# Optimization experiments

Hardware: AMD Instinct MI355X
Metric: run time of the kernel (lower is better)

The kernel has to match this reference:

```python
import jax, jax.numpy as jnp
import numpy as np

B, T, C, H = 2, 2048, 2048, 16
HD = C // H  # head_dim = 128


def setup_inputs() -> dict:
    key = jax.random.key(0)
    k1, k2, k3 = jax.random.split(key, 3)
    x = jax.random.normal(k1, (B, T, C), dtype=jnp.float32)
    # causal mask: positions with mask==0 are blocked (masked_fill(mask==0, -inf))
    mask = jnp.tril(jnp.ones((T, T), dtype=bool))[None, None]  # [1,1,T,T]
    W_qkv = jax.random.normal(k2, (C, 3 * C), dtype=jnp.float32) * (C ** -0.5)
    W_proj = jax.random.normal(k3, (C, C), dtype=jnp.float32) * (C ** -0.5)
    b_proj = jnp.zeros((C,), dtype=jnp.float32)
    return {"x": x, "mask": mask, "W_qkv": W_qkv, "W_proj": W_proj, "b_proj": b_proj}


def reference(x, mask, W_qkv, W_proj, b_proj):
    # QKV projection (Linear, bias=False)
    qkv = jnp.einsum('btc,cd->btd', x, W_qkv)            # [B,T,3C]
    qkv = qkv.reshape(B, T, 3, H, HD)
    q = qkv[:, :, 0].transpose(0, 2, 1, 3)               # [B,H,T,HD]
    k = qkv[:, :, 1].transpose(0, 2, 1, 3)
    v = qkv[:, :, 2].transpose(0, 2, 1, 3)
    # scaled dot-product attention (dropout is identity in eval)
    att = jnp.einsum('bhqd,bhkd->bhqk', q, k) / jnp.sqrt(jnp.float32(HD))
    att = jnp.where(mask, att, -jnp.inf)
    att = jax.nn.softmax(att, axis=-1)
    y = jnp.einsum('bhqk,bhkd->bhqd', att, v)            # [B,H,T,HD]
    y = y.transpose(0, 2, 1, 3).reshape(B, T, C)
    return jnp.einsum('btc,cd->btd', y, W_proj) + b_proj
```

## Files before the change

### kernel.cpp

```cpp
#include <hip/hip_runtime.h>
#include <hip/hip_bf16.h>

#define B_  2
#define T_  2048
#define C_  2048
#define H_  16
#define HD_ 128

using bf16x8 = __attribute__((ext_vector_type(8))) __bf16;
using f32x4  = __attribute__((ext_vector_type(4))) float;

__device__ __forceinline__ unsigned short f2bs(float f) {
    __hip_bfloat16 h = __float2bfloat16(f);
    return __builtin_bit_cast(unsigned short, h);
}

__device__ __forceinline__ void gload_lds16(const unsigned short* g, unsigned short* l) {
    __builtin_amdgcn_global_load_lds(
        (const __attribute__((address_space(1))) unsigned int*)g,
        (__attribute__((address_space(3))) unsigned int*)l, 16, 0, 0);
}

__global__ __launch_bounds__(256) void k_prep(const float* __restrict__ x,
                                              unsigned short* __restrict__ XB,
                                              const float* __restrict__ Wqkv,
                                              unsigned short* __restrict__ WQKVT,
                                              const float* __restrict__ Wproj,
                                              unsigned short* __restrict__ WPROJT) {
    __shared__ unsigned short t[64][65];
    int blk = blockIdx.x;
    int tid = threadIdx.x;
    if (blk < 8192) {
        int i = blk * 256 + tid;
        float4 v = reinterpret_cast<const float4*>(x)[i];
        ushort4 o;
        o.x = f2bs(v.x); o.y = f2bs(v.y); o.z = f2bs(v.z); o.w = f2bs(v.w);
        reinterpret_cast<ushort4*>(XB)[i] = o;
        return;
    }
    const float* in;
    unsigned short* out;
    int K = 2048, N, bx, by;
    if (blk < 11264) {
        in = Wqkv; out = WQKVT; N = 6144;
        bx = (blk - 8192) % 96; by = (blk - 8192) / 96;
    } else {
        in = Wproj; out = WPROJT; N = 2048;
        bx = (blk - 11264) % 32; by = (blk - 11264) / 32;
    }
    int k0 = by * 64, n0 = bx * 64;
#pragma unroll
    for (int p = 0; p < 4; ++p) {
        int idx = p * 256 + tid;
        int r = idx >> 4, c = (idx & 15) << 2;
        float4 v = *reinterpret_cast<const float4*>(in + (long)(k0 + r) * N + n0 + c);
        t[r][c] = f2bs(v.x); t[r][c + 1] = f2bs(v.y);
        t[r][c + 2] = f2bs(v.z); t[r][c + 3] = f2bs(v.w);
    }
    __syncthreads();
#pragma unroll
    for (int p = 0; p < 4; ++p) {
        int idx = p * 256 + tid;
        int r = idx >> 4, c = (idx & 15) << 2;
        ushort4 o;
        o.x = t[c][r]; o.y = t[c + 1][r]; o.z = t[c + 2][r]; o.w = t[c + 3][r];
        *reinterpret_cast<ushort4*>(out + (long)(n0 + r) * K + k0 + c) = o;
    }
}

template <int MODE>
__global__ __launch_bounds__(256, 2) void k_gemm(const unsigned short* __restrict__ A,
                                                 const unsigned short* __restrict__ Bt,
                                                 int M, int N, int K,
                                                 unsigned short* __restrict__ qkv,
                                                 float* __restrict__ out,
                                                 const float* __restrict__ bias) {
    __shared__ __align__(16) unsigned short lA[2][128 * 32];
    __shared__ __align__(16) unsigned short lB[2][128 * 32];

    int tid = threadIdx.x;
    int wave = tid >> 6, lane = tid & 63;
    int quad = lane >> 4, l16 = lane & 15;
    int wr = (wave >> 1) * 64, wc = (wave & 1) * 64;
    int m0 = blockIdx.y * 128, n0 = blockIdx.x * 128;

    int lrow = lane >> 2;
    int lcol = (lane & 3) << 3;
    const unsigned short* gA0 = A + (long)(m0 + wave * 32 + lrow) * K + lcol;
    const unsigned short* gA1 = A + (long)(m0 + wave * 32 + 16 + lrow) * K + lcol;
    const unsigned short* gB0 = Bt + (long)(n0 + wave * 32 + lrow) * K + lcol;
    const unsigned short* gB1 = Bt + (long)(n0 + wave * 32 + 16 + lrow) * K + lcol;
    int lofs0 = wave * 1024, lofs1 = wave * 1024 + 512;

    f32x4 zero = {0.f, 0.f, 0.f, 0.f};
    f32x4 acc[4][4];
#pragma unroll
    for (int i = 0; i < 4; ++i)
#pragma unroll
        for (int j = 0; j < 4; ++j) acc[i][j] = zero;

    for (int k0 = 0; k0 < K; k0 += 64) {
        __syncthreads();
#pragma unroll
        for (int h = 0; h < 2; ++h) {
            int kk = k0 + h * 32;
            gload_lds16(gA0 + kk, &lA[h][lofs0]);
            gload_lds16(gA1 + kk, &lA[h][lofs1]);
            gload_lds16(gB0 + kk, &lB[h][lofs0]);
            gload_lds16(gB1 + kk, &lB[h][lofs1]);
        }
        __syncthreads();
#pragma unroll
        for (int h = 0; h < 2; ++h) {
            bf16x8 af[4], bfr[4];
#pragma unroll
            for (int i = 0; i < 4; ++i)
                af[i] = *reinterpret_cast<const bf16x8*>(&lA[h][(wr + i * 16 + l16) * 32 + quad * 8]);
#pragma unroll
            for (int j = 0; j < 4; ++j)
                bfr[j] = *reinterpret_cast<const bf16x8*>(&lB[h][(wc + j * 16 + l16) * 32 + quad * 8]);
#pragma unroll
            for (int i = 0; i < 4; ++i)
#pragma unroll
                for (int j = 0; j < 4; ++j)
                    acc[i][j] = __builtin_amdgcn_mfma_f32_16x16x32_bf16(af[i], bfr[j], acc[i][j], 0, 0, 0);
        }
    }

#pragma unroll
    for (int i = 0; i < 4; ++i) {
#pragma unroll
        for (int j = 0; j < 4; ++j) {
#pragma unroll
            for (int r = 0; r < 4; ++r) {
                int m = m0 + wr + i * 16 + quad * 4 + r;
                int n = n0 + wc + j * 16 + l16;
                float v = acc[i][j][r];
                if (MODE == 0) {
                    int s = n >> 11, col = n & 2047;
                    int h = col >> 7, hd = col & 127;
                    int b = m >> 11, t = m & 2047;
                    long base = (long)s * (B_ * H_ * T_ * HD_);
                    if (s == 2)
                        qkv[base + ((long)(b * H_ + h) * HD_ + hd) * T_ + t] = f2bs(v);
                    else
                        qkv[base + ((long)(b * H_ + h) * T_ + t) * HD_ + hd] = f2bs(v);
                } else {
                    out[(long)m * N + n] = v + bias[n];
                }
            }
        }
    }
}

__global__ __launch_bounds__(256, 3) void k_attn(const unsigned short* __restrict__ qkv,
                                                 unsigned short* __restrict__ y) {
    __shared__ __align__(16) unsigned short lK[4][64 * 32];
    __shared__ __align__(16) unsigned short lVt[2][128 * 32];
    __shared__ __align__(16) unsigned short lP[4][16 * 72];

    int tid = threadIdx.x;
    int wave = tid >> 6, lane = tid & 63;
    int quad = lane >> 4, l16 = lane & 15;
    int bh = blockIdx.x;
    int qb = ((int)gridDim.y - 1 - (int)blockIdx.y) * 64;

    const unsigned short* Qh = qkv + (long)bh * (T_ * HD_);
    const unsigned short* Kh = qkv + (long)(B_ * H_) * T_ * HD_ + (long)bh * (T_ * HD_);
    const unsigned short* Vt = qkv + 2L * (B_ * H_) * T_ * HD_ + (long)bh * (HD_ * T_);

    bf16x8 aQ[4];
    int qrow = qb + wave * 16 + l16;
#pragma unroll
    for (int kk = 0; kk < 4; ++kk)
        aQ[kk] = *reinterpret_cast<const bf16x8*>(Qh + (long)qrow * HD_ + kk * 32 + quad * 8);

    int lrow = lane >> 2, lcol = (lane & 3) << 3;
    const unsigned short* gK = Kh + (long)(wave * 16 + lrow) * HD_ + lcol;
    const unsigned short* gV = Vt + (long)(wave * 32 + lrow) * T_ + lcol;

    float m_s[4], l_s[4];
    f32x4 O[8];
    f32x4 zero = {0.f, 0.f, 0.f, 0.f};
#pragma unroll
    for (int r = 0; r < 4; ++r) { m_s[r] = -1e30f; l_s[r] = 0.f; }
#pragma unroll
    for (int h = 0; h < 8; ++h) O[h] = zero;

    int qmax = qb + wave * 16 + 15;
    const float scl2 = 0.1275174365f;

    for (int kb = 0; kb < qb + 64; kb += 64) {
        __syncthreads();
#pragma unroll
        for (int kk = 0; kk < 4; ++kk)
            gload_lds16(gK + kb * HD_ + kk * 32, &lK[kk][wave * 512]);
#pragma unroll
        for (int kc = 0; kc < 2; ++kc) {
            gload_lds16(gV + kb + kc * 32, &lVt[kc][wave * 1024]);
            gload_lds16(gV + 16 * T_ + kb + kc * 32, &lVt[kc][wave * 1024 + 512]);
        }
        __syncthreads();
        if (kb > qmax) continue;

        f32x4 s[4];
#pragma unroll
        for (int st = 0; st < 4; ++st) s[st] = zero;
#pragma unroll
        for (int kk = 0; kk < 4; ++kk) {
#pragma unroll
            for (int st = 0; st < 4; ++st) {
                bf16x8 b = *reinterpret_cast<const bf16x8*>(
                    &lK[kk][(st * 16 + l16) * 32 + quad * 8]);
                s[st] = __builtin_amdgcn_mfma_f32_16x16x32_bf16(aQ[kk], b, s[st], 0, 0, 0);
            }
        }

        int qg = qb + wave * 16 + quad * 4;
#pragma unroll
        for (int r = 0; r < 4; ++r) {
            int q = qg + r;
            float x[4];
#pragma unroll
            for (int st = 0; st < 4; ++st)
                x[st] = (kb + st * 16 + l16 <= q) ? s[st][r] * scl2 : -1e30f;
            float mx = fmaxf(fmaxf(x[0], x[1]), fmaxf(x[2], x[3]));
#pragma unroll
            for (int off = 1; off < 16; off <<= 1) mx = fmaxf(mx, __shfl_xor(mx, off));
            float mn = fmaxf(m_s[r], mx);
            float al = exp2f(m_s[r] - mn);
            float p[4], ps = 0.f;
#pragma unroll
            for (int st = 0; st < 4; ++st) { p[st] = exp2f(x[st] - mn); ps += p[st]; }
            m_s[r] = mn;
            l_s[r] = l_s[r] * al + ps;
            int row = quad * 4 + r;
#pragma unroll
            for (int st = 0; st < 4; ++st)
                lP[wave][row * 72 + st * 16 + l16] = f2bs(p[st]);
#pragma unroll
            for (int h = 0; h < 8; ++h) O[h][r] *= al;
        }

#pragma unroll
        for (int kc = 0; kc < 2; ++kc) {
            bf16x8 pf = *reinterpret_cast<const bf16x8*>(
                &lP[wave][l16 * 72 + kc * 32 + quad * 8]);
#pragma unroll
            for (int h = 0; h < 8; ++h) {
                bf16x8 vf = *reinterpret_cast<const bf16x8*>(
                    &lVt[kc][(h * 16 + l16) * 32 + quad * 8]);
                O[h] = __builtin_amdgcn_mfma_f32_16x16x32_bf16(pf, vf, O[h], 0, 0, 0);
            }
        }
    }

    int b = bh >> 4, hh = bh & 15;
#pragma unroll
    for (int r = 0; r < 4; ++r) {
        float l = l_s[r];
#pragma unroll
        for (int off = 1; off < 16; off <<= 1) l += __shfl_xor(l, off);
        float inv = 1.f / l;
        int t = qb + wave * 16 + quad * 4 + r;
#pragma unroll
        for (int h = 0; h < 8; ++h)
            y[(long)(b * T_ + t) * C_ + hh * HD_ + h * 16 + l16] = f2bs(O[h][r] * inv);
    }
}

extern "C" void kernel_launch(void* const* d_in, const int* in_sizes, int n_in,
                              void* d_out, int out_size, void* d_ws, size_t ws_size,
                              hipStream_t stream) {
    const float* x     = (const float*)d_in[0];
    const float* Wqkv  = (const float*)d_in[2];
    const float* Wproj = (const float*)d_in[3];
    const float* bproj = (const float*)d_in[4];
    float* out = (float*)d_out;

    unsigned short* XB     = (unsigned short*)d_ws;
    unsigned short* WQKVT  = XB + 8388608;
    unsigned short* WPROJT = WQKVT + 12582912;
    unsigned short* QKV    = WPROJT + 4194304;
    if (ws_size < 100663296) return;

    k_prep<<<12288, 256, 0, stream>>>(x, XB, Wqkv, WQKVT, Wproj, WPROJT);
    k_gemm<0><<<dim3(6144 / 128, 4096 / 128), 256, 0, stream>>>(XB, WQKVT, 4096, 6144, 2048,
                                                                QKV, nullptr, nullptr);
    k_attn<<<dim3(32, 32), 256, 0, stream>>>(QKV, XB);
    k_gemm<1><<<dim3(2048 / 128, 4096 / 128), 256, 0, stream>>>(XB, WPROJT, 4096, 2048, 2048,
                                                                nullptr, out, bproj);
}
```

Baseline: 405.2 us.

## Pair causal query tiles per block and double-buffer K/V loads in attention

Each attention block now handles two query tiles (qt and 31-qt) so every block does an equal amount of causal work, and the grid is halved. K and V tiles are double-buffered in LDS, so the next tile's global-to-LDS load is issued while the current tile is being computed. The causal mask is applied only on the diagonal tile, and blocks no longer loop over fully masked K tiles. The larger LDS footprint lowers the occupancy hint from 3 to 2 blocks per CU.

```diff
diff --git a/kernel.cpp b/kernel.cpp
--- a/kernel.cpp
+++ b/kernel.cpp
@@ -153,119 +153,143 @@
     }
 }
 
-__global__ __launch_bounds__(256, 3) void k_attn(const unsigned short* __restrict__ qkv,
+__global__ __launch_bounds__(256, 2) void k_attn(const unsigned short* __restrict__ qkv,
                                                  unsigned short* __restrict__ y) {
-    __shared__ __align__(16) unsigned short lK[4][64 * 32];
-    __shared__ __align__(16) unsigned short lVt[2][128 * 32];
+    __shared__ __align__(16) unsigned short lK[2][4][64 * 32];
+    __shared__ __align__(16) unsigned short lVt[2][2][128 * 32];
     __shared__ __align__(16) unsigned short lP[4][16 * 72];
 
     int tid = threadIdx.x;
     int wave = tid >> 6, lane = tid & 63;
     int quad = lane >> 4, l16 = lane & 15;
-    int bh = blockIdx.x;
-    int qb = ((int)gridDim.y - 1 - (int)blockIdx.y) * 64;
+    int pr = blockIdx.x;
+    int bh = blockIdx.y;
 
     const unsigned short* Qh = qkv + (long)bh * (T_ * HD_);
     const unsigned short* Kh = qkv + (long)(B_ * H_) * T_ * HD_ + (long)bh * (T_ * HD_);
     const unsigned short* Vt = qkv + 2L * (B_ * H_) * T_ * HD_ + (long)bh * (HD_ * T_);
 
-    bf16x8 aQ[4];
-    int qrow = qb + wave * 16 + l16;
-#pragma unroll
-    for (int kk = 0; kk < 4; ++kk)
-        aQ[kk] = *reinterpret_cast<const bf16x8*>(Qh + (long)qrow * HD_ + kk * 32 + quad * 8);
-
     int lrow = lane >> 2, lcol = (lane & 3) << 3;
     const unsigned short* gK = Kh + (long)(wave * 16 + lrow) * HD_ + lcol;
     const unsigned short* gV = Vt + (long)(wave * 32 + lrow) * T_ + lcol;
 
-    float m_s[4], l_s[4];
-    f32x4 O[8];
+    const float scl2 = 0.1275174365f;
+    int b = bh >> 4, hh = bh & 15;
     f32x4 zero = {0.f, 0.f, 0.f, 0.f};
-#pragma unroll
-    for (int r = 0; r < 4; ++r) { m_s[r] = -1e30f; l_s[r] = 0.f; }
-#pragma unroll
-    for (int h = 0; h < 8; ++h) O[h] = zero;
-
-    int qmax = qb + wave * 16 + 15;
-    const float scl2 = 0.1275174365f;
-
-    for (int kb = 0; kb < qb + 64; kb += 64) {
+
+#pragma unroll
+    for (int ph = 0; ph < 2; ++ph) {
+        int qt = ph ? pr : (31 - pr);
+        int qb = qt * 64;
+        int nt = qt + 1;
+
+        bf16x8 aQ[4];
+        int qrow = qb + wave * 16 + l16;
+#pragma unroll
+        for (int kk = 0; kk < 4; ++kk)
+            aQ[kk] = *reinterpret_cast<const bf16x8*>(Qh + (long)qrow * HD_ + kk * 32 + quad * 8);
+
+        float m_s[4], l_s[4];
+        f32x4 O[8];
+#pragma unroll
+        for (int r = 0; r < 4; ++r) { m_s[r] = -1e30f; l_s[r] = 0.f; }
+#pragma unroll
+        for (int h = 0; h < 8; ++h) O[h] = zero;
+
         __syncthreads();
 #pragma unroll
         for (int kk = 0; kk < 4; ++kk)
-            gload_lds16(gK + kb * HD_ + kk * 32, &lK[kk][wave * 512]);
+            gload_lds16(gK + kk * 32, &lK[0][kk][wave * 512]);
 #pragma unroll
         for (int kc = 0; kc < 2; ++kc) {
-            gload_lds16(gV + kb + kc * 32, &lVt[kc][wave * 1024]);
-            gload_lds16(gV + 16 * T_ + kb + kc * 32, &lVt[kc][wave * 1024 + 512]);
-        }
-        __syncthreads();
-        if (kb > qmax) continue;
-
-        f32x4 s[4];
-#pragma unroll
-        for (int st = 0; st < 4; ++st) s[st] = zero;
-#pragma unroll
-        for (int kk = 0; kk < 4; ++kk) {
-#pragma unroll
-            for (int st = 0; st < 4; ++st) {
-                bf16x8 b = *reinterpret_cast<const bf16x8*>(
-                    &lK[kk][(st * 16 + l16) * 32 + quad * 8]);
-                s[st] = __builtin_amdgcn_mfma_f32_16x16x32_bf16(aQ[kk], b, s[st], 0, 0, 0);
-            }
-        }
-
-        int qg = qb + wave * 16 + quad * 4;
+            gload_lds16(gV + kc * 32, &lVt[0][kc][wave * 1024]);
+            gload_lds16(gV + 16 * T_ + kc * 32, &lVt[0][kc][wave * 1024 + 512]);
+        }
+
+        for (int it = 0; it < nt; ++it) {
+            int buf = it & 1;
+            int kb = it * 64;
+            __syncthreads();
+            if (it + 1 < nt) {
+                int kb1 = kb + 64;
+#pragma unroll
+                for (int kk = 0; kk < 4; ++kk)
+                    gload_lds16(gK + (long)kb1 * HD_ + kk * 32, &lK[buf ^ 1][kk][wave * 512]);
+#pragma unroll
+                for (int kc = 0; kc < 2; ++kc) {
+                    gload_lds16(gV + kb1 + kc * 32, &lVt[buf ^ 1][kc][wave * 1024]);
+                    gload_lds16(gV + 16 * T_ + kb1 + kc * 32, &lVt[buf ^ 1][kc][wave * 1024 + 512]);
+                }
+            }
+
+            f32x4 s[4];
+#pragma unroll
+            for (int st = 0; st < 4; ++st) s[st] = zero;
+#pragma unroll
+            for (int kk = 0; kk < 4; ++kk) {
+#pragma unroll
+                for (int st = 0; st < 4; ++st) {
+                    bf16x8 bb = *reinterpret_cast<const bf16x8*>(
+                        &lK[buf][kk][(st * 16 + l16) * 32 + quad * 8]);
+                    s[st] = __builtin_amdgcn_mfma_f32_16x16x32_bf16(aQ[kk], bb, s[st], 0, 0, 0);
+                }
+            }
+
+            bool diag = (it == nt - 1);
+            int qg = qb + wave * 16 + quad * 4;
+#pragma unroll
+            for (int r = 0; r < 4; ++r) {
+                float x[4];
+#pragma unroll
+                for (int st = 0; st < 4; ++st) x[st] = s[st][r] * scl2;
+                if (diag) {
+                    int q = qg + r;
+#pragma unroll
+                    for (int st = 0; st < 4; ++st)
+                        if (kb + st * 16 + l16 > q) x[st] = -1e30f;
+                }
+                float mx = fmaxf(fmaxf(x[0], x[1]), fmaxf(x[2], x[3]));
+#pragma unroll
+                for (int off = 1; off < 16; off <<= 1) mx = fmaxf(mx, __shfl_xor(mx, off));
+                float mn = fmaxf(m_s[r], mx);
+                float al = exp2f(m_s[r] - mn);
+                float p[4], ps = 0.f;
+#pragma unroll
+                for (int st = 0; st < 4; ++st) { p[st] = exp2f(x[st] - mn); ps += p[st]; }
+                m_s[r] = mn;
+                l_s[r] = l_s[r] * al + ps;
+                int row = quad * 4 + r;
+#pragma unroll
+                for (int st = 0; st < 4; ++st)
+                    lP[wave][row * 72 + st * 16 + l16] = f2bs(p[st]);
+#pragma unroll
+                for (int h = 0; h < 8; ++h) O[h][r] *= al;
+            }
+
+#pragma unroll
+            for (int kc = 0; kc < 2; ++kc) {
+                bf16x8 pf = *reinterpret_cast<const bf16x8*>(
+                    &lP[wave][l16 * 72 + kc * 32 + quad * 8]);
+#pragma unroll
+                for (int h = 0; h < 8; ++h) {
+                    bf16x8 vf = *reinterpret_cast<const bf16x8*>(
+                        &lVt[buf][kc][(h * 16 + l16) * 32 + quad * 8]);
+                    O[h] = __builtin_amdgcn_mfma_f32_16x16x32_bf16(pf, vf, O[h], 0, 0, 0);
+                }
+            }
+        }
+
 #pragma unroll
         for (int r = 0; r < 4; ++r) {
-            int q = qg + r;
-            float x[4];
-#pragma unroll
-            for (int st = 0; st < 4; ++st)
-                x[st] = (kb + st * 16 + l16 <= q) ? s[st][r] * scl2 : -1e30f;
-            float mx = fmaxf(fmaxf(x[0], x[1]), fmaxf(x[2], x[3]));
-#pragma unroll
-            for (int off = 1; off < 16; off <<= 1) mx = fmaxf(mx, __shfl_xor(mx, off));
-            float mn = fmaxf(m_s[r], mx);
-            float al = exp2f(m_s[r] - mn);
-            float p[4], ps = 0.f;
-#pragma unroll
-            for (int st = 0; st < 4; ++st) { p[st] = exp2f(x[st] - mn); ps += p[st]; }
-            m_s[r] = mn;
-            l_s[r] = l_s[r] * al + ps;
-            int row = quad * 4 + r;
-#pragma unroll
-            for (int st = 0; st < 4; ++st)
-                lP[wave][row * 72 + st * 16 + l16] = f2bs(p[st]);
-#pragma unroll
-            for (int h = 0; h < 8; ++h) O[h][r] *= al;
-        }
-
-#pragma unroll
-        for (int kc = 0; kc < 2; ++kc) {
-            bf16x8 pf = *reinterpret_cast<const bf16x8*>(
-                &lP[wave][l16 * 72 + kc * 32 + quad * 8]);
-#pragma unroll
-            for (int h = 0; h < 8; ++h) {
-                bf16x8 vf = *reinterpret_cast<const bf16x8*>(
-                    &lVt[kc][(h * 16 + l16) * 32 + quad * 8]);
-                O[h] = __builtin_amdgcn_mfma_f32_16x16x32_bf16(pf, vf, O[h], 0, 0, 0);
-            }
-        }
-    }
-
-    int b = bh >> 4, hh = bh & 15;
-#pragma unroll
-    for (int r = 0; r < 4; ++r) {
-        float l = l_s[r];
-#pragma unroll
-        for (int off = 1; off < 16; off <<= 1) l += __shfl_xor(l, off);
-        float inv = 1.f / l;
-        int t = qb + wave * 16 + quad * 4 + r;
-#pragma unroll
-        for (int h = 0; h < 8; ++h)
-            y[(long)(b * T_ + t) * C_ + hh * HD_ + h * 16 + l16] = f2bs(O[h][r] * inv);
+            float l = l_s[r];
+#pragma unroll
+            for (int off = 1; off < 16; off <<= 1) l += __shfl_xor(l, off);
+            float inv = 1.f / l;
+            int t = qb + wave * 16 + quad * 4 + r;
+#pragma unroll
+            for (int h = 0; h < 8; ++h)
+                y[(long)(b * T_ + t) * C_ + hh * HD_ + h * 16 + l16] = f2bs(O[h][r] * inv);
+        }
     }
 }
 
@@ -287,7 +311,7 @@
     k_prep<<<12288, 256, 0, stream>>>(x, XB, Wqkv, WQKVT, Wproj, WPROJT);
     k_gemm<0><<<dim3(6144 / 128, 4096 / 128), 256, 0, stream>>>(XB, WQKVT, 4096, 6144, 2048,
                                                                 QKV, nullptr, nullptr);
-    k_attn<<<dim3(32, 32), 256, 0, stream>>>(QKV, XB);
+    k_attn<<<dim3(16, 32), 256, 0, stream>>>(QKV, XB);
     k_gemm<1><<<dim3(2048 / 128, 4096 / 128), 256, 0, stream>>>(XB, WPROJT, 4096, 2048, 2048,
                                                                 nullptr, out, bproj);
 }
```

New measurement: 407.1 us. Within noise of the previous version (+0.5%).
